# Kernel tuning notes

Hardware: AMD Instinct MI355X
Metric: run time of the kernel (lower is better)

## Reference

```python
import jax, jax.numpy as jnp
import numpy as np

D = 512
B, S = 4, 4096


def setup_inputs() -> dict:
    key = jax.random.key(0)
    ks = jax.random.split(key, 8)
    scale = 1.0 / np.sqrt(D)
    return {
        "x": jax.random.normal(ks[0], (B, S, D), dtype=jnp.float32),
        "bias": jax.random.normal(ks[1], (1, S, S), dtype=jnp.float32),
        "Wq_w": jax.random.normal(ks[2], (D, D), dtype=jnp.float32) * scale,
        "Wq_b": jax.random.normal(ks[3], (D,), dtype=jnp.float32) * 0.02,
        "Wk_w": jax.random.normal(ks[4], (D, D), dtype=jnp.float32) * scale,
        "Wk_b": jax.random.normal(ks[5], (D,), dtype=jnp.float32) * 0.02,
        "Wv_w": jax.random.normal(ks[6], (D, D), dtype=jnp.float32) * scale,
        "Wv_b": jax.random.normal(ks[7], (D,), dtype=jnp.float32) * 0.02,
    }


def reference(x, bias, Wq_w, Wq_b, Wk_w, Wk_b, Wv_w, Wv_b):
    # torch nn.Linear: y = x @ W.T + b
    q = jnp.einsum("bsd,ed->bse", x, Wq_w) + Wq_b
    k = jnp.einsum("bsd,ed->bse", x, Wk_w) + Wk_b
    v = jnp.einsum("bsd,ed->bse", x, Wv_w) + Wv_b
    inv_sqrt_d = jnp.asarray(1.0 / np.sqrt(D), dtype=x.dtype)
    # scores: [B, S, S] -- scale by sqrt(feature_dim) as in the original
    scores = jnp.einsum("bqd,bkd->bqk", q * inv_sqrt_d, k) + bias
    weights = jax.nn.sigmoid(scores)
    out = jnp.einsum("bqk,bkd->bqd", weights, v)
    return out
```

## Files before the change

kernel.cpp:

```cpp
#include <hip/hip_runtime.h>
#include <hip/hip_bf16.h>
#include <stdint.h>

typedef unsigned short bf16_t;
typedef __attribute__((ext_vector_type(8))) short short8;
typedef __attribute__((ext_vector_type(4))) float f32x4;

__device__ __forceinline__ bf16_t f2b(float f) {
    union { float f; uint32_t u; } v; v.f = f;
    uint32_t u = v.u;
    return (bf16_t)((u + 0x7FFFu + ((u >> 16) & 1u)) >> 16);
}

__global__ __launch_bounds__(256) void cvt_f32_bf16(const float* __restrict__ in,
                                                    bf16_t* __restrict__ out, int n4) {
    int i = blockIdx.x * blockDim.x + threadIdx.x;
    if (i >= n4) return;
    float4 f = ((const float4*)in)[i];
    ushort4 o;
    o.x = f2b(f.x); o.y = f2b(f.y); o.z = f2b(f.z); o.w = f2b(f.w);
    ((ushort4*)out)[i] = o;
}

__global__ __launch_bounds__(256) void cvt_w3(const float* __restrict__ a,
                                              const float* __restrict__ b,
                                              const float* __restrict__ c,
                                              bf16_t* __restrict__ out) {
    int i = blockIdx.x * blockDim.x + threadIdx.x;
    const int which = i >> 16;
    const int idx   = i & 65535;
    const float* src = (which == 0) ? a : (which == 1) ? b : c;
    float4 f = ((const float4*)src)[idx];
    ushort4 o;
    o.x = f2b(f.x); o.y = f2b(f.y); o.z = f2b(f.z); o.w = f2b(f.w);
    ((ushort4*)out)[i] = o;
}

__device__ __forceinline__ void lds_dma16(const void* g, void* l) {
    __builtin_amdgcn_global_load_lds(
        (const __attribute__((address_space(1))) void*)g,
        (__attribute__((address_space(3))) void*)l, 16, 0, 0);
}


__global__ __launch_bounds__(256)
void proj_all(const bf16_t* __restrict__ Xb, const bf16_t* __restrict__ Wb,
              const float* __restrict__ qb, const float* __restrict__ kb,
              const float* __restrict__ vb,
              bf16_t* __restrict__ Qb, bf16_t* __restrict__ Kb,
              bf16_t* __restrict__ Vt)
{
    __shared__ bf16_t lsA[128 * 64];
    __shared__ bf16_t lsB[128 * 64];

    const int tid  = threadIdx.x;
    const int lane = tid & 63;
    const int w    = tid >> 6;
    const int wm   = w & 1, wn = w >> 1;
    const int ll   = lane & 15;
    const int quad = lane >> 4;

    const int m0 = blockIdx.y * 128;
    const int n0 = blockIdx.x * 128;
    const int z  = blockIdx.z;

    const bf16_t* A = Xb;
    const bf16_t* B = Wb + z * 262144;

    f32x4 acc[4][4];
#pragma unroll
    for (int i = 0; i < 4; i++)
#pragma unroll
        for (int j = 0; j < 4; j++) acc[i][j] = (f32x4){0.f, 0.f, 0.f, 0.f};

    for (int k0 = 0; k0 < 512; k0 += 64) {
#pragma unroll
        for (int c = 0; c < 4; ++c) {
            const int base = (c * 4 + w) * 64;
            const int slot = base + lane;
            const int row  = slot >> 3;
            const int kc   = ((slot & 7) ^ (row & 7)) << 3;
            lds_dma16(A + (size_t)(m0 + row) * 512 + k0 + kc, (char*)lsA + base * 16);
            lds_dma16(B + (size_t)(n0 + row) * 512 + k0 + kc, (char*)lsB + base * 16);
        }
        __syncthreads();

#pragma unroll
        for (int t = 0; t < 2; t++) {
            short8 af[4], bf[4];
#pragma unroll
            for (int i = 0; i < 4; i++) {
                const int ri = wm * 64 + i * 16 + ll;
                const int rj = wn * 64 + i * 16 + ll;
                af[i] = *(const short8*)(lsA + ri * 64 + (((t * 4 + quad) ^ (ll & 7)) << 3));
                bf[i] = *(const short8*)(lsB + rj * 64 + (((t * 4 + quad) ^ (ll & 7)) << 3));
            }
#pragma unroll
            for (int i = 0; i < 4; i++)
#pragma unroll
                for (int j = 0; j < 4; j++)
                    acc[i][j] = __builtin_amdgcn_mfma_f32_16x16x32_bf16(af[i], bf[j], acc[i][j], 0, 0, 0);
        }
        __syncthreads();
    }

    const float inv = 0.044194173824159216f;
#pragma unroll
    for (int i = 0; i < 4; i++) {
#pragma unroll
        for (int j = 0; j < 4; j++) {
            const int col  = n0 + wn * 64 + j * 16 + ll;
            const int rowb = m0 + wm * 64 + i * 16 + quad * 4;
            f32x4 a = acc[i][j];
            if (z == 0) {
                const float bv = qb[col];
#pragma unroll
                for (int r = 0; r < 4; r++)
                    Qb[(size_t)(rowb + r) * 512 + col] = f2b((a[r] + bv) * inv);
            } else if (z == 1) {
                const float bv = kb[col];
#pragma unroll
                for (int r = 0; r < 4; r++)
                    Kb[(size_t)(rowb + r) * 512 + col] = f2b(a[r] + bv);
            } else {
                const float bv = vb[col];
                const int b = rowb >> 12;
                const int s = rowb & 4095;
                ushort4 pk;
                pk.x = f2b(a[0] + bv);
                pk.y = f2b(a[1] + bv);
                pk.z = f2b(a[2] + bv);
                pk.w = f2b(a[3] + bv);
                *(ushort4*)(Vt + ((size_t)b * 512 + col) * 4096 + s) = pk;
            }
        }
    }
}

__global__ __launch_bounds__(256)
void scores_sig(const bf16_t* __restrict__ Qb, const bf16_t* __restrict__ Kb,
                const float* __restrict__ bias, bf16_t* __restrict__ P)
{
    __shared__ bf16_t lsA[128 * 64];
    __shared__ bf16_t lsB[128 * 64];

    const int tid  = threadIdx.x;
    const int lane = tid & 63;
    const int w    = tid >> 6;
    const int wm   = w & 1, wn = w >> 1;
    const int ll   = lane & 15;
    const int quad = lane >> 4;

    const int bx  = blockIdx.x;
    const int z   = bx & 3;
    const int t_  = bx >> 2;
    const int sup = t_ >> 5;
    const int win = t_ & 31;
    const int m0  = ((sup >> 2) * 4 + (win & 3)) * 128;
    const int n0  = ((sup & 3) * 8 + (win >> 2)) * 128;

    const bf16_t* A = Qb + (size_t)z * 2097152;
    const bf16_t* B = Kb + (size_t)z * 2097152;
    bf16_t* out = P + (size_t)z * 16777216;

    f32x4 acc[4][4];
#pragma unroll
    for (int i = 0; i < 4; i++)
#pragma unroll
        for (int j = 0; j < 4; j++) acc[i][j] = (f32x4){0.f, 0.f, 0.f, 0.f};

    for (int k0 = 0; k0 < 512; k0 += 64) {
#pragma unroll
        for (int c = 0; c < 4; ++c) {
            const int base = (c * 4 + w) * 64;
            const int slot = base + lane;
            const int row  = slot >> 3;
            const int kc   = ((slot & 7) ^ (row & 7)) << 3;
            lds_dma16(A + (size_t)(m0 + row) * 512 + k0 + kc, (char*)lsA + base * 16);
            lds_dma16(B + (size_t)(n0 + row) * 512 + k0 + kc, (char*)lsB + base * 16);
        }
        __syncthreads();

#pragma unroll
        for (int t = 0; t < 2; t++) {
            short8 af[4], bf[4];
#pragma unroll
            for (int i = 0; i < 4; i++) {
                const int ri = wm * 64 + i * 16 + ll;
                const int rj = wn * 64 + i * 16 + ll;
                af[i] = *(const short8*)(lsA + ri * 64 + (((t * 4 + quad) ^ (ll & 7)) << 3));
                bf[i] = *(const short8*)(lsB + rj * 64 + (((t * 4 + quad) ^ (ll & 7)) << 3));
            }
#pragma unroll
            for (int i = 0; i < 4; i++)
#pragma unroll
                for (int j = 0; j < 4; j++)
                    acc[i][j] = __builtin_amdgcn_mfma_f32_16x16x32_bf16(af[i], bf[j], acc[i][j], 0, 0, 0);
        }
        __syncthreads();
    }

#pragma unroll
    for (int i = 0; i < 4; i++) {
#pragma unroll
        for (int j = 0; j < 4; j++) {
            const int col  = n0 + wn * 64 + j * 16 + ll;
            const int rowb = m0 + wm * 64 + i * 16 + quad * 4;
            f32x4 a = acc[i][j];
#pragma unroll
            for (int r = 0; r < 4; r++) {
                const int row = rowb + r;
                const float v = a[r] + bias[(size_t)row * 4096 + col];
                const float p = __builtin_amdgcn_rcpf(1.f + __expf(-v));
                out[(size_t)row * 4096 + col] = (bf16_t)(__float_as_uint(p) >> 16);
            }
        }
    }
}

__global__ __launch_bounds__(256)
void pv_gemm(const bf16_t* __restrict__ P, const bf16_t* __restrict__ Vt,
             float* __restrict__ outg)
{
    __shared__ bf16_t lsA[64 * 64];
    __shared__ bf16_t lsB[256 * 64];

    const int tid  = threadIdx.x;
    const int lane = tid & 63;
    const int w    = tid >> 6;
    const int wn   = w;
    const int ll   = lane & 15;
    const int quad = lane >> 4;

    const int n0 = blockIdx.x * 256;
    const int m0 = blockIdx.y * 64;
    const int z  = blockIdx.z;

    const bf16_t* A = P + (size_t)z * 16777216;
    const bf16_t* B = Vt + (size_t)z * 2097152;
    float* out = outg + (size_t)z * 2097152;

    f32x4 acc[4][4];
#pragma unroll
    for (int i = 0; i < 4; i++)
#pragma unroll
        for (int j = 0; j < 4; j++) acc[i][j] = (f32x4){0.f, 0.f, 0.f, 0.f};

    for (int k0 = 0; k0 < 4096; k0 += 64) {
#pragma unroll
        for (int c = 0; c < 2; ++c) {
            const int base = (c * 4 + w) * 64;
            const int slot = base + lane;
            const int row  = slot >> 3;
            const int kc   = ((slot & 7) ^ (row & 7)) << 3;
            lds_dma16(A + (size_t)(m0 + row) * 4096 + k0 + kc, (char*)lsA + base * 16);
        }
#pragma unroll
        for (int c = 0; c < 8; ++c) {
            const int base = (c * 4 + w) * 64;
            const int slot = base + lane;
            const int row  = slot >> 3;
            const int kc   = ((slot & 7) ^ (row & 7)) << 3;
            lds_dma16(B + (size_t)(n0 + row) * 4096 + k0 + kc, (char*)lsB + base * 16);
        }
        __syncthreads();

#pragma unroll
        for (int t = 0; t < 2; t++) {
            short8 af[4], bf[4];
#pragma unroll
            for (int i = 0; i < 4; i++) {
                const int ri = i * 16 + ll;
                const int rj = wn * 64 + i * 16 + ll;
                af[i] = *(const short8*)(lsA + ri * 64 + (((t * 4 + quad) ^ (ll & 7)) << 3));
                bf[i] = *(const short8*)(lsB + rj * 64 + (((t * 4 + quad) ^ (ll & 7)) << 3));
            }
#pragma unroll
            for (int i = 0; i < 4; i++)
#pragma unroll
                for (int j = 0; j < 4; j++)
                    acc[i][j] = __builtin_amdgcn_mfma_f32_16x16x32_bf16(af[i], bf[j], acc[i][j], 0, 0, 0);
        }
        __syncthreads();
    }

#pragma unroll
    for (int i = 0; i < 4; i++) {
#pragma unroll
        for (int j = 0; j < 4; j++) {
            const int col  = n0 + wn * 64 + j * 16 + ll;
            const int rowb = m0 + i * 16 + quad * 4;
            f32x4 a = acc[i][j];
#pragma unroll
            for (int r = 0; r < 4; r++)
                out[(size_t)(rowb + r) * 512 + col] = a[r];
        }
    }
}

extern "C" void kernel_launch(void* const* d_in, const int* in_sizes, int n_in,
                              void* d_out, int out_size, void* d_ws, size_t ws_size,
                              hipStream_t stream) {
    (void)in_sizes; (void)n_in; (void)out_size; (void)ws_size;
    const float* x    = (const float*)d_in[0];
    const float* bias = (const float*)d_in[1];
    const float* Wq_w = (const float*)d_in[2];
    const float* Wq_b = (const float*)d_in[3];
    const float* Wk_w = (const float*)d_in[4];
    const float* Wk_b = (const float*)d_in[5];
    const float* Wv_w = (const float*)d_in[6];
    const float* Wv_b = (const float*)d_in[7];
    float* out = (float*)d_out;

    bf16_t* Xb = (bf16_t*)d_ws;
    bf16_t* Wb = Xb + (size_t)16384 * 512;
    bf16_t* Qb = Wb + (size_t)3 * 512 * 512;
    bf16_t* Kb = Qb + (size_t)16384 * 512;
    bf16_t* Vt = Kb + (size_t)16384 * 512;
    bf16_t* P  = Vt + (size_t)16384 * 512;

    cvt_f32_bf16<<<8192, 256, 0, stream>>>(x, Xb, 2097152);
    cvt_w3<<<768, 256, 0, stream>>>(Wq_w, Wk_w, Wv_w, Wb);

    proj_all<<<dim3(4, 128, 3), 256, 0, stream>>>(Xb, Wb, Wq_b, Wk_b, Wv_b,
                                                  Qb, Kb, Vt);
    scores_sig<<<4096, 256, 0, stream>>>(Qb, Kb, bias, P);
    pv_gemm<<<dim3(2, 64, 4), 256, 0, stream>>>(P, Vt, out);
}
```

Measured before the change: 437.6 us.

## Stage GEMM epilogues through LDS, remap blocks per XCD, widen PV tile

The projection and score kernels now write their output tiles into swizzled LDS per wave and then store 16-byte vectors to global memory, replacing the strided 2-byte stores. Block indices are remapped so that blocks sharing an input (the same X rows or the same batch) land on the same XCD, which should improve L2 reuse. The PV GEMM grows to 512 threads covering all 512 output columns, so each block reads its P rows once instead of twice. The costs are an extra LDS round trip with a barrier, and a larger LDS footprint and thread count in pv_gemm, which may reduce occupancy.

```diff
diff --git a/kernel.cpp b/kernel.cpp
--- a/kernel.cpp
+++ b/kernel.cpp
@@ -3,6 +3,7 @@
 #include <stdint.h>
 
 typedef unsigned short bf16_t;
+typedef __attribute__((ext_vector_type(4))) short s4v;
 typedef __attribute__((ext_vector_type(8))) short short8;
 typedef __attribute__((ext_vector_type(4))) float f32x4;
 
@@ -50,8 +51,9 @@
               bf16_t* __restrict__ Qb, bf16_t* __restrict__ Kb,
               bf16_t* __restrict__ Vt)
 {
-    __shared__ bf16_t lsA[128 * 64];
-    __shared__ bf16_t lsB[128 * 64];
+    __shared__ __align__(16) bf16_t lds[16384];
+    bf16_t* lsA = lds;
+    bf16_t* lsB = lds + 8192;
 
     const int tid  = threadIdx.x;
     const int lane = tid & 63;
@@ -60,9 +62,14 @@
     const int ll   = lane & 15;
     const int quad = lane >> 4;
 
-    const int m0 = blockIdx.y * 128;
-    const int n0 = blockIdx.x * 128;
-    const int z  = blockIdx.z;
+    const int bid   = blockIdx.x;
+    const int x     = bid & 7;
+    const int g     = bid >> 3;
+    const int mi    = x * 16 + g / 12;
+    const int inner = g % 12;
+    const int m0 = mi * 128;
+    const int n0 = (inner & 3) * 128;
+    const int z  = inner >> 2;
 
     const bf16_t* A = Xb;
     const bf16_t* B = Wb + z * 262144;
@@ -104,35 +111,65 @@
         __syncthreads();
     }
 
+    bf16_t* wbuf = lds + w * 4096;
     const float inv = 0.044194173824159216f;
-#pragma unroll
-    for (int i = 0; i < 4; i++) {
+
+    if (z != 2) {
+        const float* bptr = (z == 0) ? qb : kb;
+        const float scl   = (z == 0) ? inv : 1.0f;
 #pragma unroll
         for (int j = 0; j < 4; j++) {
-            const int col  = n0 + wn * 64 + j * 16 + ll;
-            const int rowb = m0 + wm * 64 + i * 16 + quad * 4;
-            f32x4 a = acc[i][j];
-            if (z == 0) {
-                const float bv = qb[col];
-#pragma unroll
-                for (int r = 0; r < 4; r++)
-                    Qb[(size_t)(rowb + r) * 512 + col] = f2b((a[r] + bv) * inv);
-            } else if (z == 1) {
-                const float bv = kb[col];
-#pragma unroll
-                for (int r = 0; r < 4; r++)
-                    Kb[(size_t)(rowb + r) * 512 + col] = f2b(a[r] + bv);
-            } else {
-                const float bv = vb[col];
-                const int b = rowb >> 12;
-                const int s = rowb & 4095;
-                ushort4 pk;
-                pk.x = f2b(a[0] + bv);
-                pk.y = f2b(a[1] + bv);
-                pk.z = f2b(a[2] + bv);
-                pk.w = f2b(a[3] + bv);
-                *(ushort4*)(Vt + ((size_t)b * 512 + col) * 4096 + s) = pk;
-            }
+            const int colL = j * 16 + ll;
+            const float bv = bptr[n0 + wn * 64 + colL];
+#pragma unroll
+            for (int i = 0; i < 4; i++) {
+                f32x4 a = acc[i][j];
+#pragma unroll
+                for (int r = 0; r < 4; r++) {
+                    const int rowL = i * 16 + quad * 4 + r;
+                    wbuf[rowL * 64 + (colL ^ ((rowL & 7) << 3))] = f2b((a[r] + bv) * scl);
+                }
+            }
+        }
+        __syncthreads();
+        bf16_t* dst = (z == 0) ? Qb : Kb;
+        const int rowg0 = m0 + wm * 64;
+        const int colg0 = n0 + wn * 64;
+#pragma unroll
+        for (int k = 0; k < 8; k++) {
+            const int rowL = (lane >> 3) + k * 8;
+            const int c0   = (lane & 7) * 8;
+            short8 vv = *(const short8*)(wbuf + rowL * 64 + (c0 ^ ((rowL & 7) << 3)));
+            *(short8*)(dst + (size_t)(rowg0 + rowL) * 512 + colg0 + c0) = vv;
+        }
+    } else {
+#pragma unroll
+        for (int j = 0; j < 4; j++) {
+            const int d = j * 16 + ll;
+            const float bv = vb[n0 + wn * 64 + d];
+#pragma unroll
+            for (int i = 0; i < 4; i++) {
+                f32x4 a = acc[i][j];
+                s4v pk;
+                pk[0] = (short)f2b(a[0] + bv);
+                pk[1] = (short)f2b(a[1] + bv);
+                pk[2] = (short)f2b(a[2] + bv);
+                pk[3] = (short)f2b(a[3] + bv);
+                const int sB = i * 16 + quad * 4;
+                *(s4v*)(wbuf + d * 64 + (sB ^ ((d & 7) << 3))) = pk;
+            }
+        }
+        __syncthreads();
+        const int rowg0 = m0 + wm * 64;
+        const int b  = rowg0 >> 12;
+        const int s0 = rowg0 & 4095;
+        const int d0 = n0 + wn * 64;
+#pragma unroll
+        for (int k = 0; k < 8; k++) {
+            const int dL = (lane >> 3) + k * 8;
+            const int c0 = (lane & 7) * 8;
+            short8 vv = *(const short8*)(wbuf + dL * 64 + (c0 ^ ((dL & 7) << 3)));
+            *(short8*)(Vt + ((size_t)b * 512 + d0 + dL) * 4096 + s0 + c0) = vv;
         }
     }
 }
@@ -141,8 +178,9 @@
 void scores_sig(const bf16_t* __restrict__ Qb, const bf16_t* __restrict__ Kb,
                 const float* __restrict__ bias, bf16_t* __restrict__ P)
 {
-    __shared__ bf16_t lsA[128 * 64];
-    __shared__ bf16_t lsB[128 * 64];
+    __shared__ __align__(16) bf16_t lds[16384];
+    bf16_t* lsA = lds;
+    bf16_t* lsB = lds + 8192;
 
     const int tid  = threadIdx.x;
     const int lane = tid & 63;
@@ -151,9 +189,11 @@
     const int ll   = lane & 15;
     const int quad = lane >> 4;
 
-    const int bx  = blockIdx.x;
-    const int z   = bx & 3;
-    const int t_  = bx >> 2;
+    const int bid = blockIdx.x;
+    const int x   = bid & 7;
+    const int g   = bid >> 3;
+    const int z   = g & 3;
+    const int t_  = x + ((g >> 2) << 3);
     const int sup = t_ >> 5;
     const int win = t_ & 31;
     const int m0  = ((sup >> 2) * 4 + (win & 3)) * 128;
@@ -200,41 +240,54 @@
         __syncthreads();
     }
 
+    bf16_t* wbuf = lds + w * 4096;
 #pragma unroll
     for (int i = 0; i < 4; i++) {
 #pragma unroll
         for (int j = 0; j < 4; j++) {
-            const int col  = n0 + wn * 64 + j * 16 + ll;
+            const int colL = j * 16 + ll;
+            const int colg = n0 + wn * 64 + colL;
             const int rowb = m0 + wm * 64 + i * 16 + quad * 4;
             f32x4 a = acc[i][j];
 #pragma unroll
             for (int r = 0; r < 4; r++) {
-                const int row = rowb + r;
-                const float v = a[r] + bias[(size_t)row * 4096 + col];
+                const float v = a[r] + bias[(size_t)(rowb + r) * 4096 + colg];
                 const float p = __builtin_amdgcn_rcpf(1.f + __expf(-v));
-                out[(size_t)row * 4096 + col] = (bf16_t)(__float_as_uint(p) >> 16);
-            }
-        }
-    }
-}
-
-__global__ __launch_bounds__(256)
+                const int rowL = i * 16 + quad * 4 + r;
+                wbuf[rowL * 64 + (colL ^ ((rowL & 7) << 3))] = (bf16_t)(__float_as_uint(p) >> 16);
+            }
+        }
+    }
+    __syncthreads();
+    const int rowg0 = m0 + wm * 64;
+    const int colg0 = n0 + wn * 64;
+#pragma unroll
+    for (int k = 0; k < 8; k++) {
+        const int rowL = (lane >> 3) + k * 8;
+        const int c0   = (lane & 7) * 8;
+        short8 vv = *(const short8*)(wbuf + rowL * 64 + (c0 ^ ((rowL & 7) << 3)));
+        *(short8*)(out + (size_t)(rowg0 + rowL) * 4096 + colg0 + c0) = vv;
+    }
+}
+
+__global__ __launch_bounds__(512)
 void pv_gemm(const bf16_t* __restrict__ P, const bf16_t* __restrict__ Vt,
              float* __restrict__ outg)
 {
-    __shared__ bf16_t lsA[64 * 64];
-    __shared__ bf16_t lsB[256 * 64];
+    __shared__ __align__(16) bf16_t lsA[64 * 64];
+    __shared__ __align__(16) bf16_t lsB[512 * 64];
 
     const int tid  = threadIdx.x;
     const int lane = tid & 63;
     const int w    = tid >> 6;
-    const int wn   = w;
     const int ll   = lane & 15;
     const int quad = lane >> 4;
 
-    const int n0 = blockIdx.x * 256;
-    const int m0 = blockIdx.y * 64;
-    const int z  = blockIdx.z;
+    const int bid = blockIdx.x;
+    const int x   = bid & 7;
+    const int g   = bid >> 3;
+    const int z   = x >> 1;
+    const int m0  = ((x & 1) * 32 + g) * 64;
 
     const bf16_t* A = P + (size_t)z * 16777216;
     const bf16_t* B = Vt + (size_t)z * 2097152;
@@ -247,9 +300,8 @@
         for (int j = 0; j < 4; j++) acc[i][j] = (f32x4){0.f, 0.f, 0.f, 0.f};
 
     for (int k0 = 0; k0 < 4096; k0 += 64) {
-#pragma unroll
-        for (int c = 0; c < 2; ++c) {
-            const int base = (c * 4 + w) * 64;
+        {
+            const int base = w * 64;
             const int slot = base + lane;
             const int row  = slot >> 3;
             const int kc   = ((slot & 7) ^ (row & 7)) << 3;
@@ -257,11 +309,11 @@
         }
 #pragma unroll
         for (int c = 0; c < 8; ++c) {
-            const int base = (c * 4 + w) * 64;
+            const int base = (c * 8 + w) * 64;
             const int slot = base + lane;
             const int row  = slot >> 3;
             const int kc   = ((slot & 7) ^ (row & 7)) << 3;
-            lds_dma16(B + (size_t)(n0 + row) * 4096 + k0 + kc, (char*)lsB + base * 16);
+            lds_dma16(B + (size_t)row * 4096 + k0 + kc, (char*)lsB + base * 16);
         }
         __syncthreads();
 
@@ -271,7 +323,7 @@
 #pragma unroll
             for (int i = 0; i < 4; i++) {
                 const int ri = i * 16 + ll;
-                const int rj = wn * 64 + i * 16 + ll;
+                const int rj = w * 64 + i * 16 + ll;
                 af[i] = *(const short8*)(lsA + ri * 64 + (((t * 4 + quad) ^ (ll & 7)) << 3));
                 bf[i] = *(const short8*)(lsB + rj * 64 + (((t * 4 + quad) ^ (ll & 7)) << 3));
             }
@@ -288,7 +340,7 @@
     for (int i = 0; i < 4; i++) {
 #pragma unroll
         for (int j = 0; j < 4; j++) {
-            const int col  = n0 + wn * 64 + j * 16 + ll;
+            const int col  = w * 64 + j * 16 + ll;
             const int rowb = m0 + i * 16 + quad * 4;
             f32x4 a = acc[i][j];
 #pragma unroll
@@ -322,8 +374,7 @@
     cvt_f32_bf16<<<8192, 256, 0, stream>>>(x, Xb, 2097152);
     cvt_w3<<<768, 256, 0, stream>>>(Wq_w, Wk_w, Wv_w, Wb);
 
-    proj_all<<<dim3(4, 128, 3), 256, 0, stream>>>(Xb, Wb, Wq_b, Wk_b, Wv_b,
-                                                  Qb, Kb, Vt);
+    proj_all<<<1536, 256, 0, stream>>>(Xb, Wb, Wq_b, Wk_b, Wv_b, Qb, Kb, Vt);
     scores_sig<<<4096, 256, 0, stream>>>(Qb, Kb, bias, P);
-    pv_gemm<<<dim3(2, 64, 4), 256, 0, stream>>>(P, Vt, out);
-}
+    pv_gemm<<<256, 512, 0, stream>>>(P, Vt, out);
+}
```

Result: slower. 455.1 us (+4.0%).
